# Performance work log

Hardware: AMD Instinct MI355X
Metric: run time of the kernel (lower is better)

The kernel has to match this reference:

```python
import jax, jax.numpy as jnp
import numpy as np

V, H, I, E, K, L = 32000, 1024, 4096, 8, 2, 2
B, S = 1, 2048

def setup_inputs() -> dict:
    key = jax.random.key(0)
    ks = jax.random.split(key, 8)
    s = 0.02
    d = {}
    d["input_ids"] = jax.random.randint(ks[0], (B, S), 0, V)
    d["emb"] = jax.random.normal(ks[1], (V, H), jnp.float32) * s
    d["router_w"] = jax.random.normal(ks[2], (L, E, H), jnp.float32) * s
    d["router_b"] = jnp.zeros((L, E), jnp.float32)
    d["fc1_w"] = jax.random.normal(ks[3], (L, E, I, H), jnp.float32) * s
    d["fc1_b"] = jnp.zeros((L, E, I), jnp.float32)
    d["fc2_w"] = jax.random.normal(ks[4], (L, E, H, I), jnp.float32) * s
    d["fc2_b"] = jnp.zeros((L, E, H), jnp.float32)
    d["ln_g"] = jnp.ones((L, H), jnp.float32)
    d["ln_b"] = jnp.zeros((L, H), jnp.float32)
    d["head_w"] = jax.random.normal(ks[5], (V, H), jnp.float32) * s
    d["head_b"] = jnp.zeros((V,), jnp.float32)
    return d

def _moe_layer(h, rw, rb, f1w, f1b, f2w, f2b, g, b):
    # h: [T,H]
    T = h.shape[0]
    logits = h @ rw.T + rb                                  # [T,E]
    top_w, sel = jax.lax.top_k(logits, K)                   # [T,K]
    top_w = jax.nn.softmax(top_w, axis=-1)
    sel_oh = sel[None, :, :] == jnp.arange(E)[:, None, None]  # [E,T,K]
    mask = sel_oh.any(-1)                                     # [E,T]
    w_tok = jnp.sum(jnp.where(sel_oh, top_w[None], 0.0), -1)  # [E,T]
    cnt = mask.sum(-1).astype(h.dtype)                        # [E]
    # faithful to source: per-expert SCALAR weight = mean of routing weights of routed tokens
    scal = jnp.where(cnt > 0, w_tok.sum(-1) / jnp.maximum(cnt, 1.0), 0.0)  # [E]
    a = jax.nn.gelu(jnp.einsum('th,eih->eti', h, f1w) + f1b[:, None, :], approximate=False)
    eo = jnp.einsum('eti,ehi->eth', a, f2w) + f2b[:, None, :]             # [E,T,H]
    out = jnp.einsum('et,eth->th', mask.astype(h.dtype) * scal[:, None], eo)
    mu = out.mean(-1, keepdims=True)
    var = out.var(-1, keepdims=True)
    out = (out - mu) / jnp.sqrt(var + 1e-5) * g + b
    counts = sel_oh.sum((1, 2)).astype(h.dtype)
    aux = jnp.mean((counts - T / E) ** 2) * 0.01
    return out, aux

def reference(input_ids, emb, router_w, router_b, fc1_w, fc1_b, fc2_w, fc2_b, ln_g, ln_b, head_w, head_b):
    h = emb[input_ids].reshape(-1, H)   # [T,H]
    aux_total = jnp.float32(0.0)
    for l in range(L):
        h, aux = _moe_layer(h, router_w[l], router_b[l], fc1_w[l], fc1_b[l],
                            fc2_w[l], fc2_b[l], ln_g[l], ln_b[l])
        aux_total = aux_total + aux
    logits = h @ head_w.T + head_b
    return logits.reshape(B, S, V), aux_total
```

## Files before the change

### kernel.cpp

```cpp
#include <hip/hip_runtime.h>
#include <math.h>

constexpr int kT = 2048;
constexpr int kH = 1024;
constexpr int kI = 4096;
constexpr int kE = 8;
constexpr int kV = 32000;
constexpr int kL = 2;
constexpr int kR = 4096;
constexpr int kRp = 5120;
constexpr int kSK = 4;
constexpr int kNB = kR / 128 + kE - 1;

typedef __attribute__((ext_vector_type(4))) float f32x4;
typedef __attribute__((ext_vector_type(8))) short bf16x8;

__device__ inline unsigned cvtpk(float lo, float hi) {
  unsigned r;
  asm("v_cvt_pk_bf16_f32 %0, %1, %2" : "=v"(r) : "v"(lo), "v"(hi));
  return r;
}

__device__ inline unsigned short f2bf(float x) {
  union { float f; unsigned u; } c; c.f = x;
  unsigned u = c.u;
  u += 0x7FFFu + ((u >> 16) & 1u);
  return (unsigned short)(u >> 16);
}

__device__ inline void dec2(float x, float y,
                            unsigned& p1, unsigned& p2, unsigned& p3) {
  unsigned ux = __float_as_uint(x), uy = __float_as_uint(y);
  unsigned x1 = ux & 0xFFFF0000u, y1 = uy & 0xFFFF0000u;
  float rx = x - __uint_as_float(x1), ry = y - __uint_as_float(y1);
  unsigned x2 = __float_as_uint(rx) & 0xFFFF0000u;
  unsigned y2 = __float_as_uint(ry) & 0xFFFF0000u;
  float sx = rx - __uint_as_float(x2), sy = ry - __uint_as_float(y2);
  p1 = (x1 >> 16) | y1;
  p2 = (x2 >> 16) | y2;
  p3 = (__float_as_uint(sx) >> 16) | (__float_as_uint(sy) & 0xFFFF0000u);
}

__device__ inline void dec1(float x, unsigned short& b1, unsigned short& b2,
                            unsigned short& b3) {
  unsigned u = __float_as_uint(x);
  unsigned x1 = u & 0xFFFF0000u;
  float r = x - __uint_as_float(x1);
  unsigned x2 = __float_as_uint(r) & 0xFFFF0000u;
  float s = r - __uint_as_float(x2);
  b1 = (unsigned short)(x1 >> 16);
  b2 = (unsigned short)(x2 >> 16);
  b3 = (unsigned short)(__float_as_uint(s) >> 16);
}

__device__ inline int swz(int e) { return e ^ (((e >> 6) & 3) << 3); }


__global__ void gather_k(const int* __restrict__ ids, const float* __restrict__ emb,
                         float* __restrict__ h) {
  int t = blockIdx.x;
  int id = ids[t];
  const float4* src = (const float4*)(emb + (size_t)id * kH);
  float4* dst = (float4*)(h + (size_t)t * kH);
  dst[threadIdx.x] = src[threadIdx.x];
}

__global__ void router_k(const float* __restrict__ h, const float* __restrict__ rw,
                         const float* __restrict__ rb, float* __restrict__ logits) {
  int t = blockIdx.x;
  int lg = threadIdx.x & 31;
  int e = threadIdx.x >> 5;
  const float* hr = h + (size_t)t * kH;
  const float* wr = rw + (size_t)e * kH;
  float p = 0.f;
  for (int k = lg * 4; k < kH; k += 128) {
    float4 a = *(const float4*)(hr + k);
    float4 b = *(const float4*)(wr + k);
    p += a.x * b.x + a.y * b.y + a.z * b.z + a.w * b.w;
  }
  for (int o = 16; o > 0; o >>= 1) p += __shfl_down(p, o, 32);
  if (lg == 0) logits[t * kE + e] = p + rb[e];
}

__global__ void topk_k(const float* __restrict__ logits, int* __restrict__ sel,
                       float* __restrict__ w_sum, int* __restrict__ cnt) {
  int t = blockIdx.x * blockDim.x + threadIdx.x;
  if (t >= kT) return;
  float v[8];
#pragma unroll
  for (int e = 0; e < 8; e++) v[e] = logits[t * 8 + e];
  int e1 = 0; float v1 = v[0];
#pragma unroll
  for (int e = 1; e < 8; e++) if (v[e] > v1) { v1 = v[e]; e1 = e; }
  int e2 = -1; float v2 = -3.4e38f;
#pragma unroll
  for (int e = 0; e < 8; e++) if (e != e1 && v[e] > v2) { v2 = v[e]; e2 = e; }
  float z = expf(v2 - v1);
  float w1 = 1.f / (1.f + z);
  float w2 = z * w1;
  sel[t * 2] = e1;
  sel[t * 2 + 1] = e2;
  atomicAdd(&w_sum[e1], w1);
  atomicAdd(&w_sum[e2], w2);
  atomicAdd(&cnt[e1], 1);
  atomicAdd(&cnt[e2], 1);
}

__global__ void finalize_k(const int* __restrict__ cnt, const float* __restrict__ w_sum,
                           float* __restrict__ scal, int* __restrict__ off,
                           int* __restrict__ fill, float* __restrict__ aux,
                           int* __restrict__ blk_e, int* __restrict__ blk_m) {
  if (threadIdx.x == 0) {
    int o = 0;
    float a = 0.f;
    for (int e = 0; e < 8; e++) {
      off[e] = o;
      o += (cnt[e] + 127) & ~127;
      fill[e] = 0;
      int c = cnt[e];
      scal[e] = c > 0 ? w_sum[e] / (float)c : 0.f;
      float d = (float)c - 256.f;
      a += d * d;
    }
    aux[0] += 0.01f * (a * 0.125f);
    int nb = 0;
    for (int e = 0; e < 8; e++)
      for (int m = 0; m < cnt[e]; m += 128) { blk_e[nb] = e; blk_m[nb] = m; nb++; }
    for (int i = nb; i < kNB; i++) { blk_e[i] = -1; blk_m[i] = 0; }
  }
}

__global__ void scatter_k(const int* __restrict__ sel, const int* __restrict__ off,
                          int* __restrict__ fill, int* __restrict__ list,
                          int* __restrict__ pos) {
  int t = blockIdx.x * blockDim.x + threadIdx.x;
  if (t >= kT) return;
#pragma unroll
  for (int s = 0; s < 2; s++) {
    int e = sel[t * 2 + s];
    int p = atomicAdd(&fill[e], 1);
    int slot = off[e] + p;
    list[slot] = t;
    pos[t * 2 + s] = slot;
  }
}

__global__ void cvt_k(const float* __restrict__ src, unsigned short* __restrict__ dst, long n) {
  long i = ((long)blockIdx.x * 256 + threadIdx.x) * 8;
  if (i >= n) return;
  float4 a = *(const float4*)(src + i);
  float4 b = *(const float4*)(src + i + 4);
  uint4 pk;
  pk.x = (unsigned)f2bf(a.x) | ((unsigned)f2bf(a.y) << 16);
  pk.y = (unsigned)f2bf(a.z) | ((unsigned)f2bf(a.w) << 16);
  pk.z = (unsigned)f2bf(b.x) | ((unsigned)f2bf(b.y) << 16);
  pk.w = (unsigned)f2bf(b.z) | ((unsigned)f2bf(b.w) << 16);
  *(uint4*)(dst + i) = pk;
}

__global__ void hdec_k(const float* __restrict__ h, const int* __restrict__ list,
                       unsigned short* __restrict__ hp, long PH) {
  int s = blockIdx.x * 2 + (threadIdx.x >> 7);
  int k8 = (threadIdx.x & 127) * 8;
  int t = list[s];
  const float* src = h + (size_t)t * kH + k8;
  float4 a = *(const float4*)(src);
  float4 b = *(const float4*)(src + 4);
  float x[8];
  *(float4*)&x[0] = a; *(float4*)&x[4] = b;
  unsigned q1[4], q2[4], q3[4];
#pragma unroll
  for (int i = 0; i < 4; i++) dec2(x[2 * i], x[2 * i + 1], q1[i], q2[i], q3[i]);
  int sw = (s >> 1) & 3;
  int colp = (k8 & ~31) | ((((k8 >> 3) & 3) ^ sw) << 3);
  long base = (long)s * kH + colp;
  *(uint4*)(hp + 0 * PH + base) = *(uint4*)q1;
  *(uint4*)(hp + 1 * PH + base) = *(uint4*)q2;
  *(uint4*)(hp + 2 * PH + base) = *(uint4*)q3;
}

__global__ void combine_ln_k(const float* __restrict__ ccomp, const int* __restrict__ pos,
                             float* __restrict__ h, const float* __restrict__ g,
                             const float* __restrict__ b) {
  int t = blockIdx.x;
  int s0 = pos[t * 2], s1 = pos[t * 2 + 1];
  int k = threadIdx.x * 4;
  float4 v = {0.f, 0.f, 0.f, 0.f};
#pragma unroll
  for (int kc = 0; kc < kSK; kc++) {
    const float* base = ccomp + (size_t)kc * ((size_t)kRp * kH);
    float4 a = *(const float4*)(base + (size_t)s0 * kH + k);
    float4 c = *(const float4*)(base + (size_t)s1 * kH + k);
    v.x += a.x + c.x; v.y += a.y + c.y; v.z += a.z + c.z; v.w += a.w + c.w;
  }
  float s = v.x + v.y + v.z + v.w;
  float sq = v.x * v.x + v.y * v.y + v.z * v.z + v.w * v.w;
  for (int o = 32; o > 0; o >>= 1) {
    s += __shfl_down(s, o);
    sq += __shfl_down(sq, o);
  }
  __shared__ float ss[4], sqs[4];
  int wave = threadIdx.x >> 6, lane = threadIdx.x & 63;
  if (lane == 0) { ss[wave] = s; sqs[wave] = sq; }
  __syncthreads();
  __shared__ float mu, inv;
  if (threadIdx.x == 0) {
    float st = ss[0] + ss[1] + ss[2] + ss[3];
    float sqt = sqs[0] + sqs[1] + sqs[2] + sqs[3];
    float m = st / (float)kH;
    float var = sqt / (float)kH - m * m;
    mu = m;
    inv = 1.f / sqrtf(var + 1e-5f);
  }
  __syncthreads();
  float4 gg = *(const float4*)(g + k);
  float4 bb = *(const float4*)(b + k);
  float4 o;
  o.x = (v.x - mu) * inv * gg.x + bb.x;
  o.y = (v.y - mu) * inv * gg.y + bb.y;
  o.z = (v.z - mu) * inv * gg.z + bb.z;
  o.w = (v.w - mu) * inv * gg.w + bb.w;
  *(float4*)(h + (size_t)t * kH + k) = o;
}

__global__ void aux_write_k(float* __restrict__ out, const float* __restrict__ aux) {
  out[(size_t)kT * kV] = aux[0];
}

template <int MODE>
__launch_bounds__(256)
__global__ void tgemm_k(const unsigned short* __restrict__ Ap, long PA, int ldA,
                        const float* __restrict__ Bbase,
                        const float* __restrict__ bias,
                        float* __restrict__ Cout,
                        unsigned short* __restrict__ Cp, long PCp,
                        const int* __restrict__ off,
                        const int* __restrict__ cnt,
                        const float* __restrict__ scal,
                        const int* __restrict__ blk_e,
                        const int* __restrict__ blk_m,
                        int N, int Kd) {
  const int e = blk_e[blockIdx.y];
  if (e < 0) return;
  const int m0 = blk_m[blockIdx.y];
  const int M = cnt[e];
  int nb = blockIdx.x, kc = 0;
  if constexpr (MODE == 1) { nb = blockIdx.x >> 2; kc = blockIdx.x & 3; }
  const int n0 = nb * 128;
  const int roff = off[e];
  const float* Bp = Bbase + (size_t)e * (size_t)N * (size_t)Kd;
  const float* be = bias + (size_t)e * (size_t)N;
  const int kBeg = (MODE == 1) ? kc * (Kd >> 2) : 0;
  const int kEnd = (MODE == 1) ? kBeg + (Kd >> 2) : Kd;

  __shared__ __align__(16) unsigned short AsL[2][3][128 * 32];
  __shared__ __align__(16) unsigned short BsL[3][128 * 32];

  const int tid = threadIdx.x, w = tid >> 6, l = tid & 63;

  long abase[2];
#pragma unroll
  for (int i = 0; i < 2; i++) {
    int r = w * 16 + i * 64 + (l >> 2);
    int gr = m0 + r; if (gr > M - 1) gr = M - 1;
    abase[i] = (long)(roff + gr) * ldA + (l & 3) * 8;
  }

  const int srow = tid >> 1, scolh = (tid & 1) * 16;
  const float* bsrc = Bp + (size_t)(n0 + srow) * (size_t)Kd + scolh;
  const int e0 = srow * 32 + scolh;
  const int s0b = swz(e0), s1b = swz(e0 + 8);

  f32x4 acc[4][4] = {};
  const int wm = w >> 1, wn = w & 1;
  const int fr = l & 15, fk = (l >> 4) * 8;
  const int cola = ((l >> 4) ^ ((fr >> 1) & 3)) * 8;

  float4 rvb[4];
  unsigned qb1[8], qb2[8], qb3[8];

#define LOADB(K0)                                      \
  _Pragma("unroll") for (int i = 0; i < 4; i++)        \
    rvb[i] = *(const float4*)(bsrc + (K0) + i * 4);

#define DECB()                                                 \
  {                                                            \
    float xb[16];                                              \
    *(float4*)&xb[0] = rvb[0]; *(float4*)&xb[4] = rvb[1];      \
    *(float4*)&xb[8] = rvb[2]; *(float4*)&xb[12] = rvb[3];     \
    _Pragma("unroll") for (int i = 0; i < 8; i++)              \
      dec2(xb[2 * i], xb[2 * i + 1], qb1[i], qb2[i], qb3[i]);  \
  }

#define ISSUE_A(K0, PBUF)                                                      \
  _Pragma("unroll") for (int pp = 0; pp < 3; pp++)                             \
    _Pragma("unroll") for (int ii = 0; ii < 2; ii++)                           \
      __builtin_amdgcn_global_load_lds(                                        \
          (const __attribute__((address_space(1))) unsigned int*)(const void*) \
              (Ap + (long)pp * PA + abase[ii] + (K0)),                         \
          (__attribute__((address_space(3))) unsigned int*)(void*)             \
              (&AsL[PBUF][pp][(w * 16 + ii * 64) * 32]),                       \
          16, 0, 0);

  LOADB(kBeg);
  DECB();
  ISSUE_A(kBeg, 0);
  int p = 0;

  for (int k0 = kBeg; k0 < kEnd; k0 += 32) {
    *(uint4*)&BsL[0][s0b] = *(uint4*)&qb1[0]; *(uint4*)&BsL[0][s1b] = *(uint4*)&qb1[4];
    *(uint4*)&BsL[1][s0b] = *(uint4*)&qb2[0]; *(uint4*)&BsL[1][s1b] = *(uint4*)&qb2[4];
    *(uint4*)&BsL[2][s0b] = *(uint4*)&qb3[0]; *(uint4*)&BsL[2][s1b] = *(uint4*)&qb3[4];
    __syncthreads();
    const bool more = (k0 + 32 < kEnd);
    if (more) {
      ISSUE_A(k0 + 32, (p ^ 1));
      LOADB(k0 + 32);
    }

    bf16x8 bf1[4], bf2[4], bf3[4];
#pragma unroll
    for (int bn = 0; bn < 4; bn++) {
      int se = swz((wn * 64 + bn * 16 + fr) * 32 + fk);
      bf1[bn] = *(const bf16x8*)(&BsL[0][se]);
      bf2[bn] = *(const bf16x8*)(&BsL[1][se]);
      bf3[bn] = *(const bf16x8*)(&BsL[2][se]);
    }
#pragma unroll
    for (int am = 0; am < 4; am++) {
      int ra = (wm * 64 + am * 16 + fr) * 32 + cola;
      bf16x8 a1 = *(const bf16x8*)(&AsL[p][0][ra]);
      bf16x8 a2 = *(const bf16x8*)(&AsL[p][1][ra]);
      bf16x8 a3 = *(const bf16x8*)(&AsL[p][2][ra]);
#pragma unroll
      for (int bn = 0; bn < 4; bn++) {
        f32x4 c = acc[am][bn];
        c = __builtin_amdgcn_mfma_f32_16x16x32_bf16(a3, bf1[bn], c, 0, 0, 0);
        c = __builtin_amdgcn_mfma_f32_16x16x32_bf16(a2, bf2[bn], c, 0, 0, 0);
        c = __builtin_amdgcn_mfma_f32_16x16x32_bf16(a1, bf3[bn], c, 0, 0, 0);
        c = __builtin_amdgcn_mfma_f32_16x16x32_bf16(a2, bf1[bn], c, 0, 0, 0);
        c = __builtin_amdgcn_mfma_f32_16x16x32_bf16(a1, bf2[bn], c, 0, 0, 0);
        c = __builtin_amdgcn_mfma_f32_16x16x32_bf16(a1, bf1[bn], c, 0, 0, 0);
        acc[am][bn] = c;
      }
    }
    if (more) DECB();
    __syncthreads();
    p ^= 1;
  }
#undef LOADB
#undef DECB
#undef ISSUE_A

  const int r0 = (l >> 4) * 4, cc = l & 15;
#pragma unroll
  for (int am = 0; am < 4; am++) {
#pragma unroll
    for (int bn = 0; bn < 4; bn++) {
      int gn = n0 + wn * 64 + bn * 16 + cc;
      float bv;
      if constexpr (MODE == 1) bv = (kc == 0) ? be[gn] : 0.f;
      else bv = be[gn];
#pragma unroll
      for (int j = 0; j < 4; j++) {
        int gm = m0 + wm * 64 + am * 16 + r0 + j;
        if (gm >= M) continue;
        float v = acc[am][bn][j] + bv;
        if constexpr (MODE == 0) {
          float g = 0.5f * v * (1.f + erff(v * 0.70710678118654752f));
          unsigned short b1, b2, b3;
          dec1(g, b1, b2, b3);
          int sw2 = ((r0 + j) >> 1) & 3;
          int colp = (gn & ~31) | ((((gn >> 3) & 3) ^ sw2) << 3) | (gn & 7);
          long base = (long)(roff + gm) * N + colp;
          Cp[0 * PCp + base] = b1;
          Cp[1 * PCp + base] = b2;
          Cp[2 * PCp + base] = b3;
        } else {
          Cout[(size_t)kc * ((size_t)kRp * kH) + (size_t)(roff + gm) * (size_t)N + gn] =
              scal[e] * v;
        }
      }
    }
  }
}

template <int MODE>
__launch_bounds__(256)
__global__ void wgemm_k(const unsigned short* __restrict__ Abase, int ldA,
                        const unsigned short* __restrict__ Bbase,
                        const float* __restrict__ bias,
                        float* __restrict__ Cout,
                        unsigned short* __restrict__ Cbf,
                        const int* __restrict__ list,
                        const int* __restrict__ off,
                        const int* __restrict__ cnt,
                        const float* __restrict__ scal,
                        const int* __restrict__ blk_e,
                        const int* __restrict__ blk_m,
                        int N, int Kd) {
  const int e = blk_e[blockIdx.x];
  if (e < 0) return;
  const int m0 = blk_m[blockIdx.x];
  const int M = cnt[e];
  int nb = blockIdx.y, kc = 0;
  if constexpr (MODE == 1) { nb = blockIdx.y >> 2; kc = blockIdx.y & 3; }
  const int n0 = nb * 128;
  const int roff = off[e];
  const unsigned short* Bp = Bbase + (size_t)e * (size_t)N * (size_t)Kd;
  const float* be = bias + (size_t)e * (size_t)N;
  const int kBeg = (MODE == 1) ? kc * (Kd >> 2) : 0;
  const int kEnd = (MODE == 1) ? kBeg + (Kd >> 2) : Kd;

  __shared__ __align__(16) unsigned short As[128 * 64];
  __shared__ __align__(16) unsigned short Bs[128 * 64];

  const int tid = threadIdx.x, w = tid >> 6, l = tid & 63;

  const unsigned short* asrc[4];
  const unsigned short* bsrc[4];
#pragma unroll
  for (int i = 0; i < 4; i++) {
    int r = w * 8 + i * 32 + (l >> 3);
    int gr = m0 + r; if (gr > M - 1) gr = M - 1;
    long grow;
    if constexpr (MODE == 0) grow = list[roff + gr];
    else grow = roff + gr;
    asrc[i] = Abase + grow * (long)ldA + (l & 7) * 8;
    bsrc[i] = Bp + (size_t)(n0 + r) * (size_t)Kd + (l & 7) * 8;
  }

  f32x4 acc[4][4] = {};
  const int wm = w >> 1, wn = w & 1;
  const int fr = l & 15, fk = (l >> 4) * 8;

  for (int k0 = kBeg; k0 < kEnd; k0 += 64) {
#pragma unroll
    for (int i = 0; i < 4; i++) {
      __builtin_amdgcn_global_load_lds(
          (const __attribute__((address_space(1))) unsigned int*)(const void*)(asrc[i] + k0),
          (__attribute__((address_space(3))) unsigned int*)(void*)(As + w * 512 + i * 2048),
          16, 0, 0);
      __builtin_amdgcn_global_load_lds(
          (const __attribute__((address_space(1))) unsigned int*)(const void*)(bsrc[i] + k0),
          (__attribute__((address_space(3))) unsigned int*)(void*)(Bs + w * 512 + i * 2048),
          16, 0, 0);
    }
    __syncthreads();
#pragma unroll
    for (int ks = 0; ks < 2; ks++) {
      bf16x8 af[4], bfr[4];
#pragma unroll
      for (int am = 0; am < 4; am++)
        af[am] = *(const bf16x8*)(As + (wm * 64 + am * 16 + fr) * 64 + ks * 32 + fk);
#pragma unroll
      for (int bn = 0; bn < 4; bn++)
        bfr[bn] = *(const bf16x8*)(Bs + (wn * 64 + bn * 16 + fr) * 64 + ks * 32 + fk);
#pragma unroll
      for (int am = 0; am < 4; am++)
#pragma unroll
        for (int bn = 0; bn < 4; bn++)
          acc[am][bn] = __builtin_amdgcn_mfma_f32_16x16x32_bf16(af[am], bfr[bn], acc[am][bn], 0, 0, 0);
    }
    __syncthreads();
  }

  const int r0 = (l >> 4) * 4, cc = l & 15;
#pragma unroll
  for (int am = 0; am < 4; am++) {
#pragma unroll
    for (int bn = 0; bn < 4; bn++) {
      int gn = n0 + wn * 64 + bn * 16 + cc;
      float bv;
      if constexpr (MODE == 1) bv = (kc == 0) ? be[gn] : 0.f;
      else bv = be[gn];
#pragma unroll
      for (int j = 0; j < 4; j++) {
        int gm = m0 + wm * 64 + am * 16 + r0 + j;
        if (gm >= M) continue;
        float v = acc[am][bn][j] + bv;
        if constexpr (MODE == 0) {
          float g = 0.5f * v * (1.f + erff(v * 0.70710678118654752f));
          Cbf[(size_t)(roff + gm) * (size_t)N + gn] = f2bf(g);
        } else {
          Cout[(size_t)kc * ((size_t)kRp * kH) + (size_t)(roff + gm) * (size_t)N + gn] =
              scal[e] * v;
        }
      }
    }
  }
}

__launch_bounds__(256)
__global__ void hgemm_k(const unsigned short* __restrict__ hbf,
                        const float* __restrict__ Bw,
                        const float* __restrict__ bias,
                        float* __restrict__ Cout) {
  int bx = blockIdx.x, by = blockIdx.y;
  {
    int lin = by * gridDim.x + bx;
    int nwg = gridDim.x * gridDim.y;
    int q = nwg >> 3, r = nwg & 7;
    int xcd = lin & 7, idx = lin >> 3;
    int swzb = (xcd < r ? xcd * (q + 1) : r * (q + 1) + (xcd - r) * q) + idx;
    bx = swzb % gridDim.x;
    by = swzb / gridDim.x;
  }
  const int m0 = bx * 128;
  const int n0 = by * 128;

  __shared__ __align__(16) unsigned short As[128 * 64];
  __shared__ __align__(16) unsigned short Bs[128 * 64];

  const int tid = threadIdx.x, w = tid >> 6, l = tid & 63;

  const unsigned short* asrc[4];
  const float* bsrc[4];
#pragma unroll
  for (int i = 0; i < 4; i++) {
    int r = w * 8 + i * 32 + (l >> 3);
    asrc[i] = hbf + (size_t)(m0 + r) * kH + (l & 7) * 8;
    bsrc[i] = Bw + (size_t)(n0 + r) * kH + (l & 7) * 8;
  }
  const int ldstB = w * 512 + (l >> 3) * 64 + (((l & 7) ^ (l >> 3)) * 8);

  f32x4 acc[4][4] = {};
  const int wm = w >> 1, wn = w & 1;
  const int fr = l & 15, fk = (l >> 4) * 8;
  const int col0 = (((l >> 4) + 0) ^ (l & 7)) * 8;
  const int col1 = (((l >> 4) + 4) ^ (l & 7)) * 8;

  float4 rb[4][2];
#define LOADB(K0)                                            \
  _Pragma("unroll") for (int i = 0; i < 4; i++) {            \
    rb[i][0] = *(const float4*)(bsrc[i] + (K0));             \
    rb[i][1] = *(const float4*)(bsrc[i] + (K0) + 4);         \
  }

  LOADB(0);

  for (int k0 = 0; k0 < kH; k0 += 64) {
#pragma unroll
    for (int i = 0; i < 4; i++) {
      __builtin_amdgcn_global_load_lds(
          (const __attribute__((address_space(1))) unsigned int*)(const void*)(asrc[i] + k0),
          (__attribute__((address_space(3))) unsigned int*)(void*)(As + w * 512 + i * 2048),
          16, 0, 0);
      uint4 pb;
      pb.x = cvtpk(rb[i][0].x, rb[i][0].y);
      pb.y = cvtpk(rb[i][0].z, rb[i][0].w);
      pb.z = cvtpk(rb[i][1].x, rb[i][1].y);
      pb.w = cvtpk(rb[i][1].z, rb[i][1].w);
      *(uint4*)(Bs + ldstB + i * 2048) = pb;
    }
    __syncthreads();
    if (k0 + 64 < kH) LOADB(k0 + 64);
#pragma unroll
    for (int ks = 0; ks < 2; ks++) {
      const int ck = ks ? col1 : col0;
      bf16x8 af[4], bfr[4];
#pragma unroll
      for (int am = 0; am < 4; am++)
        af[am] = *(const bf16x8*)(As + (wm * 64 + am * 16 + fr) * 64 + ks * 32 + fk);
#pragma unroll
      for (int bn = 0; bn < 4; bn++)
        bfr[bn] = *(const bf16x8*)(Bs + (wn * 64 + bn * 16 + fr) * 64 + ck);
#pragma unroll
      for (int am = 0; am < 4; am++)
#pragma unroll
        for (int bn = 0; bn < 4; bn++)
          acc[am][bn] = __builtin_amdgcn_mfma_f32_16x16x32_bf16(af[am], bfr[bn], acc[am][bn], 0, 0, 0);
    }
    __syncthreads();
  }
#undef LOADB

  const int r0 = (l >> 4) * 4, cc = l & 15;
#pragma unroll
  for (int am = 0; am < 4; am++) {
#pragma unroll
    for (int bn = 0; bn < 4; bn++) {
      int gn = n0 + wn * 64 + bn * 16 + cc;
      float bv = bias[gn];
#pragma unroll
      for (int j = 0; j < 4; j++) {
        int gm = m0 + wm * 64 + am * 16 + r0 + j;
        Cout[(size_t)gm * (size_t)kV + gn] = acc[am][bn][j] + bv;
      }
    }
  }
}


extern "C" void kernel_launch(void* const* d_in, const int* in_sizes, int n_in,
                              void* d_out, int out_size, void* d_ws, size_t ws_size,
                              hipStream_t stream) {
  (void)in_sizes; (void)n_in; (void)out_size; (void)ws_size;
  const int* ids = (const int*)d_in[0];
  const float* emb = (const float*)d_in[1];
  const float* router_w = (const float*)d_in[2];
  const float* router_b = (const float*)d_in[3];
  const float* fc1_w = (const float*)d_in[4];
  const float* fc1_b = (const float*)d_in[5];
  const float* fc2_w = (const float*)d_in[6];
  const float* fc2_b = (const float*)d_in[7];
  const float* ln_g = (const float*)d_in[8];
  const float* ln_b = (const float*)d_in[9];
  const float* head_w = (const float*)d_in[10];
  const float* head_b = (const float*)d_in[11];
  float* out = (float*)d_out;

  float* ws_f = (float*)d_ws;
  float* h       = ws_f;
  float* logits  = h + (size_t)kT * kH;
  float* w_sum   = logits + (size_t)kT * kE;
  float* scal    = w_sum + kE;
  float* aux     = scal + kE;
  int* sel  = (int*)(aux + 1);
  int* cnt  = sel + 2 * kT;
  int* off  = cnt + kE;
  int* fill = off + kE;
  int* list = fill + kE;
  int* pos  = list + kRp;
  int* blk_e = pos + 2 * kT;
  int* blk_m = blk_e + kNB;
  unsigned short* h_bf = (unsigned short*)(blk_m + kNB);

  const long PA_h = (long)kRp * kH;
  const long PA_a = (long)kRp * kI;
  unsigned short* ap = (unsigned short*)out;
  unsigned short* hp = ap + 3 * PA_a;
  float* c_comp = (float*)(hp + 3 * PA_h);
  unsigned short* a_bf = (unsigned short*)out;
  unsigned short* wbf = a_bf + (size_t)kRp * kI;

  hipMemsetAsync(aux, 0, sizeof(float), stream);
  gather_k<<<kT, 256, 0, stream>>>(ids, emb, h);

  for (int l = 0; l < kL; l++) {
    hipMemsetAsync(w_sum, 0, kE * sizeof(float), stream);
    hipMemsetAsync(cnt, 0, kE * sizeof(int), stream);
    hipMemsetAsync(list, 0, kRp * sizeof(int), stream);
    router_k<<<kT, 256, 0, stream>>>(h, router_w + (size_t)l * kE * kH,
                                     router_b + (size_t)l * kE, logits);
    topk_k<<<kT / 256, 256, 0, stream>>>(logits, sel, w_sum, cnt);
    finalize_k<<<1, 64, 0, stream>>>(cnt, w_sum, scal, off, fill, aux, blk_e, blk_m);
    scatter_k<<<kT / 256, 256, 0, stream>>>(sel, off, fill, list, pos);

    if (l == 0) {
      hdec_k<<<kRp / 2, 256, 0, stream>>>(h, list, hp, PA_h);
      tgemm_k<0><<<dim3(kI / 128, kNB), 256, 0, stream>>>(
          hp, PA_h, kH, fc1_w + (size_t)l * kE * kI * kH, fc1_b + (size_t)l * kE * kI,
          nullptr, ap, PA_a, off, cnt, scal, blk_e, blk_m, kI, kH);
      tgemm_k<1><<<dim3((kH / 128) * kSK, kNB), 256, 0, stream>>>(
          ap, PA_a, kI, fc2_w + (size_t)l * kE * kH * kI, fc2_b + (size_t)l * kE * kH,
          c_comp, nullptr, 0, off, cnt, scal, blk_e, blk_m, kH, kI);
    } else {
      cvt_k<<<(int)(((long)kT * kH) / 2048), 256, 0, stream>>>(h, h_bf, (long)kT * kH);
      cvt_k<<<(int)(((long)kE * kI * kH) / 2048), 256, 0, stream>>>(
          fc1_w + (size_t)l * kE * kI * kH, wbf, (long)kE * kI * kH);
      wgemm_k<0><<<dim3(kNB, kI / 128), 256, 0, stream>>>(
          h_bf, kH, wbf, fc1_b + (size_t)l * kE * kI,
          nullptr, a_bf, list, off, cnt, scal, blk_e, blk_m, kI, kH);
      cvt_k<<<(int)(((long)kE * kH * kI) / 2048), 256, 0, stream>>>(
          fc2_w + (size_t)l * kE * kH * kI, wbf, (long)kE * kH * kI);
      wgemm_k<1><<<dim3(kNB, (kH / 128) * kSK), 256, 0, stream>>>(
          a_bf, kI, wbf, fc2_b + (size_t)l * kE * kH,
          c_comp, nullptr, list, off, cnt, scal, blk_e, blk_m, kH, kI);
    }

    combine_ln_k<<<kT, 256, 0, stream>>>(c_comp, pos, h,
                                         ln_g + (size_t)l * kH, ln_b + (size_t)l * kH);
  }

  cvt_k<<<(int)(((long)kT * kH) / 2048), 256, 0, stream>>>(h, h_bf, (long)kT * kH);
  hgemm_k<<<dim3(kT / 128, kV / 128), 256, 0, stream>>>(h_bf, head_w, head_b, out);

  aux_write_k<<<1, 1, 0, stream>>>(out, aux);
}
```

Measured before the change: 1.396 ms.

## Fuse bf16 output into LayerNorm and add bf16-weight head GEMM

The combine+LayerNorm kernel now also writes a bf16 copy of the hidden state, which removes the separate float-to-bf16 conversion kernels before the layer-1 FC1 and before the LM head. When the workspace is large enough, the head weight is converted to bf16 once per call. A new head GEMM then streams both operands in bf16 through global_load_lds into LDS with XCD-aware block swizzling. This trades an extra pass over the 128MB fp32 head weight for half-width operand traffic in the main GEMM. The new path depends on ws_size, and the old hgemm_k path is kept as a fallback.

```diff
diff --git a/kernel.cpp b/kernel.cpp
--- a/kernel.cpp
+++ b/kernel.cpp
@@ -180,8 +180,8 @@
 }
 
 __global__ void combine_ln_k(const float* __restrict__ ccomp, const int* __restrict__ pos,
-                             float* __restrict__ h, const float* __restrict__ g,
-                             const float* __restrict__ b) {
+                             float* __restrict__ h, unsigned short* __restrict__ hbf,
+                             const float* __restrict__ g, const float* __restrict__ b) {
   int t = blockIdx.x;
   int s0 = pos[t * 2], s1 = pos[t * 2 + 1];
   int k = threadIdx.x * 4;
@@ -221,6 +221,10 @@
   o.z = (v.z - mu) * inv * gg.z + bb.z;
   o.w = (v.w - mu) * inv * gg.w + bb.w;
   *(float4*)(h + (size_t)t * kH + k) = o;
+  uint2 pk;
+  pk.x = (unsigned)f2bf(o.x) | ((unsigned)f2bf(o.y) << 16);
+  pk.y = (unsigned)f2bf(o.z) | ((unsigned)f2bf(o.w) << 16);
+  *(uint2*)(hbf + (size_t)t * kH + k) = pk;
 }
 
 __global__ void aux_write_k(float* __restrict__ out, const float* __restrict__ aux) {
@@ -591,11 +595,94 @@
   }
 }
 
+__launch_bounds__(256)
+__global__ void hgemm2_k(const unsigned short* __restrict__ hbf,
+                         const unsigned short* __restrict__ Bw,
+                         const float* __restrict__ bias,
+                         float* __restrict__ Cout) {
+  int bx = blockIdx.x, by = blockIdx.y;
+  {
+    int lin = by * gridDim.x + bx;
+    int nwg = gridDim.x * gridDim.y;
+    int q = nwg >> 3, r = nwg & 7;
+    int xcd = lin & 7, idx = lin >> 3;
+    int swzb = (xcd < r ? xcd * (q + 1) : r * (q + 1) + (xcd - r) * q) + idx;
+    bx = swzb % gridDim.x;
+    by = swzb / gridDim.x;
+  }
+  const int m0 = bx * 128;
+  const int n0 = by * 128;
+
+  __shared__ __align__(16) unsigned short As[128 * 64];
+  __shared__ __align__(16) unsigned short Bs[128 * 64];
+
+  const int tid = threadIdx.x, w = tid >> 6, l = tid & 63;
+
+  const unsigned short* asrc[4];
+  const unsigned short* bsrc[4];
+#pragma unroll
+  for (int i = 0; i < 4; i++) {
+    int r = w * 8 + i * 32 + (l >> 3);
+    asrc[i] = hbf + (size_t)(m0 + r) * kH + (l & 7) * 8;
+    bsrc[i] = Bw + (size_t)(n0 + r) * kH + (l & 7) * 8;
+  }
+
+  f32x4 acc[4][4] = {};
+  const int wm = w >> 1, wn = w & 1;
+  const int fr = l & 15, fk = (l >> 4) * 8;
+
+  for (int k0 = 0; k0 < kH; k0 += 64) {
+#pragma unroll
+    for (int i = 0; i < 4; i++) {
+      __builtin_amdgcn_global_load_lds(
+          (const __attribute__((address_space(1))) unsigned int*)(const void*)(asrc[i] + k0),
+          (__attribute__((address_space(3))) unsigned int*)(void*)(As + w * 512 + i * 2048),
+          16, 0, 0);
+      __builtin_amdgcn_global_load_lds(
+          (const __attribute__((address_space(1))) unsigned int*)(const void*)(bsrc[i] + k0),
+          (__attribute__((address_space(3))) unsigned int*)(void*)(Bs + w * 512 + i * 2048),
+          16, 0, 0);
+    }
+    __syncthreads();
+#pragma unroll
+    for (int ks = 0; ks < 2; ks++) {
+      bf16x8 af[4], bfr[4];
+#pragma unroll
+      for (int am = 0; am < 4; am++)
+        af[am] = *(const bf16x8*)(As + (wm * 64 + am * 16 + fr) * 64 + ks * 32 + fk);
+#pragma unroll
+      for (int bn = 0; bn < 4; bn++)
+        bfr[bn] = *(const bf16x8*)(Bs + (wn * 64 + bn * 16 + fr) * 64 + ks * 32 + fk);
+#pragma unroll
+      for (int am = 0; am < 4; am++)
+#pragma unroll
+        for (int bn = 0; bn < 4; bn++)
+          acc[am][bn] = __builtin_amdgcn_mfma_f32_16x16x32_bf16(af[am], bfr[bn], acc[am][bn], 0, 0, 0);
+    }
+    __syncthreads();
+  }
+
+  const int r0 = (l >> 4) * 4, cc = l & 15;
+#pragma unroll
+  for (int am = 0; am < 4; am++) {
+#pragma unroll
+    for (int bn = 0; bn < 4; bn++) {
+      int gn = n0 + wn * 64 + bn * 16 + cc;
+      float bv = bias[gn];
+#pragma unroll
+      for (int j = 0; j < 4; j++) {
+        int gm = m0 + wm * 64 + am * 16 + r0 + j;
+        Cout[(size_t)gm * (size_t)kV + gn] = acc[am][bn][j] + bv;
+      }
+    }
+  }
+}
+
 
 extern "C" void kernel_launch(void* const* d_in, const int* in_sizes, int n_in,
                               void* d_out, int out_size, void* d_ws, size_t ws_size,
                               hipStream_t stream) {
-  (void)in_sizes; (void)n_in; (void)out_size; (void)ws_size;
+  (void)in_sizes; (void)n_in; (void)out_size;
   const int* ids = (const int*)d_in[0];
   const float* emb = (const float*)d_in[1];
   const float* router_w = (const float*)d_in[2];
@@ -625,6 +712,9 @@
   int* blk_e = pos + 2 * kT;
   int* blk_m = blk_e + kNB;
   unsigned short* h_bf = (unsigned short*)(blk_m + kNB);
+  unsigned short* hw_bf = h_bf + (size_t)kT * kH;
+  size_t ws_need = ((char*)(hw_bf + (size_t)kV * kH) - (char*)d_ws);
+  bool head_bf = ws_size >= ws_need;
 
   const long PA_h = (long)kRp * kH;
   const long PA_a = (long)kRp * kI;
@@ -656,7 +746,6 @@
           ap, PA_a, kI, fc2_w + (size_t)l * kE * kH * kI, fc2_b + (size_t)l * kE * kH,
           c_comp, nullptr, 0, off, cnt, scal, blk_e, blk_m, kH, kI);
     } else {
-      cvt_k<<<(int)(((long)kT * kH) / 2048), 256, 0, stream>>>(h, h_bf, (long)kT * kH);
       cvt_k<<<(int)(((long)kE * kI * kH) / 2048), 256, 0, stream>>>(
           fc1_w + (size_t)l * kE * kI * kH, wbf, (long)kE * kI * kH);
       wgemm_k<0><<<dim3(kNB, kI / 128), 256, 0, stream>>>(
@@ -669,12 +758,16 @@
           c_comp, nullptr, list, off, cnt, scal, blk_e, blk_m, kH, kI);
     }
 
-    combine_ln_k<<<kT, 256, 0, stream>>>(c_comp, pos, h,
+    combine_ln_k<<<kT, 256, 0, stream>>>(c_comp, pos, h, h_bf,
                                          ln_g + (size_t)l * kH, ln_b + (size_t)l * kH);
   }
 
-  cvt_k<<<(int)(((long)kT * kH) / 2048), 256, 0, stream>>>(h, h_bf, (long)kT * kH);
-  hgemm_k<<<dim3(kT / 128, kV / 128), 256, 0, stream>>>(h_bf, head_w, head_b, out);
+  if (head_bf) {
+    cvt_k<<<(int)(((long)kV * kH) / 2048), 256, 0, stream>>>(head_w, hw_bf, (long)kV * kH);
+    hgemm2_k<<<dim3(kT / 128, kV / 128), 256, 0, stream>>>(h_bf, hw_bf, head_b, out);
+  } else {
+    hgemm_k<<<dim3(kT / 128, kV / 128), 256, 0, stream>>>(h_bf, head_w, head_b, out);
+  }
 
   aux_write_k<<<1, 1, 0, stream>>>(out, aux);
 }
```

After: 1.459 ms. 4.5% more time.

## Load A fragments directly from global in tgemm and fuse bf16 cast into layernorm

Applied to the files above, without the earlier changes.

The split-bf16 GEMM (tgemm) no longer stages A tiles through LDS with async global_load_lds double buffering. Each lane now reads its A fragments straight from global memory into registers, and the swizzled column layout used by the producers of hp and ap is dropped to match. Separately, combine_ln_k now also writes a bf16 copy of h, which removes two cvt_k launches. Direct global A loads cut LDS traffic and occupancy pressure, but they add uncoalesced, latency-exposed global reads inside the MFMA loop with no prefetch.

```diff
diff --git a/kernel.cpp b/kernel.cpp
--- a/kernel.cpp
+++ b/kernel.cpp
@@ -171,17 +171,15 @@
   unsigned q1[4], q2[4], q3[4];
 #pragma unroll
   for (int i = 0; i < 4; i++) dec2(x[2 * i], x[2 * i + 1], q1[i], q2[i], q3[i]);
-  int sw = (s >> 1) & 3;
-  int colp = (k8 & ~31) | ((((k8 >> 3) & 3) ^ sw) << 3);
-  long base = (long)s * kH + colp;
+  long base = (long)s * kH + k8;
   *(uint4*)(hp + 0 * PH + base) = *(uint4*)q1;
   *(uint4*)(hp + 1 * PH + base) = *(uint4*)q2;
   *(uint4*)(hp + 2 * PH + base) = *(uint4*)q3;
 }
 
 __global__ void combine_ln_k(const float* __restrict__ ccomp, const int* __restrict__ pos,
-                             float* __restrict__ h, const float* __restrict__ g,
-                             const float* __restrict__ b) {
+                             float* __restrict__ h, unsigned short* __restrict__ hbf,
+                             const float* __restrict__ g, const float* __restrict__ b) {
   int t = blockIdx.x;
   int s0 = pos[t * 2], s1 = pos[t * 2 + 1];
   int k = threadIdx.x * 4;
@@ -221,6 +219,10 @@
   o.z = (v.z - mu) * inv * gg.z + bb.z;
   o.w = (v.w - mu) * inv * gg.w + bb.w;
   *(float4*)(h + (size_t)t * kH + k) = o;
+  uint2 pk;
+  pk.x = (unsigned)f2bf(o.x) | ((unsigned)f2bf(o.y) << 16);
+  pk.y = (unsigned)f2bf(o.z) | ((unsigned)f2bf(o.w) << 16);
+  *(uint2*)(hbf + (size_t)t * kH + k) = pk;
 }
 
 __global__ void aux_write_k(float* __restrict__ out, const float* __restrict__ aux) {
@@ -253,17 +255,19 @@
   const int kBeg = (MODE == 1) ? kc * (Kd >> 2) : 0;
   const int kEnd = (MODE == 1) ? kBeg + (Kd >> 2) : Kd;
 
-  __shared__ __align__(16) unsigned short AsL[2][3][128 * 32];
   __shared__ __align__(16) unsigned short BsL[3][128 * 32];
 
   const int tid = threadIdx.x, w = tid >> 6, l = tid & 63;
 
-  long abase[2];
-#pragma unroll
-  for (int i = 0; i < 2; i++) {
-    int r = w * 16 + i * 64 + (l >> 2);
-    int gr = m0 + r; if (gr > M - 1) gr = M - 1;
-    abase[i] = (long)(roff + gr) * ldA + (l & 3) * 8;
+  const int wm = w >> 1, wn = w & 1;
+  const int fr = l & 15, fk = (l >> 4) * 8;
+
+  const unsigned short* aptr[4];
+#pragma unroll
+  for (int am = 0; am < 4; am++) {
+    int gr = m0 + wm * 64 + am * 16 + fr;
+    if (gr > M - 1) gr = M - 1;
+    aptr[am] = Ap + (long)(roff + gr) * ldA + fk;
   }
 
   const int srow = tid >> 1, scolh = (tid & 1) * 16;
@@ -272,9 +276,6 @@
   const int s0b = swz(e0), s1b = swz(e0 + 8);
 
   f32x4 acc[4][4] = {};
-  const int wm = w >> 1, wn = w & 1;
-  const int fr = l & 15, fk = (l >> 4) * 8;
-  const int cola = ((l >> 4) ^ ((fr >> 1) & 3)) * 8;
 
   float4 rvb[4];
   unsigned qb1[8], qb2[8], qb3[8];
@@ -292,20 +293,8 @@
       dec2(xb[2 * i], xb[2 * i + 1], qb1[i], qb2[i], qb3[i]);  \
   }
 
-#define ISSUE_A(K0, PBUF)                                                      \
-  _Pragma("unroll") for (int pp = 0; pp < 3; pp++)                             \
-    _Pragma("unroll") for (int ii = 0; ii < 2; ii++)                           \
-      __builtin_amdgcn_global_load_lds(                                        \
-          (const __attribute__((address_space(1))) unsigned int*)(const void*) \
-              (Ap + (long)pp * PA + abase[ii] + (K0)),                         \
-          (__attribute__((address_space(3))) unsigned int*)(void*)             \
-              (&AsL[PBUF][pp][(w * 16 + ii * 64) * 32]),                       \
-          16, 0, 0);
-
   LOADB(kBeg);
   DECB();
-  ISSUE_A(kBeg, 0);
-  int p = 0;
 
   for (int k0 = kBeg; k0 < kEnd; k0 += 32) {
     *(uint4*)&BsL[0][s0b] = *(uint4*)&qb1[0]; *(uint4*)&BsL[0][s1b] = *(uint4*)&qb1[4];
@@ -313,9 +302,14 @@
     *(uint4*)&BsL[2][s0b] = *(uint4*)&qb3[0]; *(uint4*)&BsL[2][s1b] = *(uint4*)&qb3[4];
     __syncthreads();
     const bool more = (k0 + 32 < kEnd);
-    if (more) {
-      ISSUE_A(k0 + 32, (p ^ 1));
-      LOADB(k0 + 32);
+    if (more) LOADB(k0 + 32);
+
+    bf16x8 af1[4], af2[4], af3[4];
+#pragma unroll
+    for (int am = 0; am < 4; am++) {
+      af1[am] = *(const bf16x8*)(aptr[am] + k0);
+      af2[am] = *(const bf16x8*)(aptr[am] + PA + k0);
+      af3[am] = *(const bf16x8*)(aptr[am] + 2 * PA + k0);
     }
 
     bf16x8 bf1[4], bf2[4], bf3[4];
@@ -328,29 +322,23 @@
     }
 #pragma unroll
     for (int am = 0; am < 4; am++) {
-      int ra = (wm * 64 + am * 16 + fr) * 32 + cola;
-      bf16x8 a1 = *(const bf16x8*)(&AsL[p][0][ra]);
-      bf16x8 a2 = *(const bf16x8*)(&AsL[p][1][ra]);
-      bf16x8 a3 = *(const bf16x8*)(&AsL[p][2][ra]);
 #pragma unroll
       for (int bn = 0; bn < 4; bn++) {
         f32x4 c = acc[am][bn];
-        c = __builtin_amdgcn_mfma_f32_16x16x32_bf16(a3, bf1[bn], c, 0, 0, 0);
-        c = __builtin_amdgcn_mfma_f32_16x16x32_bf16(a2, bf2[bn], c, 0, 0, 0);
-        c = __builtin_amdgcn_mfma_f32_16x16x32_bf16(a1, bf3[bn], c, 0, 0, 0);
-        c = __builtin_amdgcn_mfma_f32_16x16x32_bf16(a2, bf1[bn], c, 0, 0, 0);
-        c = __builtin_amdgcn_mfma_f32_16x16x32_bf16(a1, bf2[bn], c, 0, 0, 0);
-        c = __builtin_amdgcn_mfma_f32_16x16x32_bf16(a1, bf1[bn], c, 0, 0, 0);
+        c = __builtin_amdgcn_mfma_f32_16x16x32_bf16(af3[am], bf1[bn], c, 0, 0, 0);
+        c = __builtin_amdgcn_mfma_f32_16x16x32_bf16(af2[am], bf2[bn], c, 0, 0, 0);
+        c = __builtin_amdgcn_mfma_f32_16x16x32_bf16(af1[am], bf3[bn], c, 0, 0, 0);
+        c = __builtin_amdgcn_mfma_f32_16x16x32_bf16(af2[am], bf1[bn], c, 0, 0, 0);
+        c = __builtin_amdgcn_mfma_f32_16x16x32_bf16(af1[am], bf2[bn], c, 0, 0, 0);
+        c = __builtin_amdgcn_mfma_f32_16x16x32_bf16(af1[am], bf1[bn], c, 0, 0, 0);
         acc[am][bn] = c;
       }
     }
     if (more) DECB();
     __syncthreads();
-    p ^= 1;
   }
 #undef LOADB
 #undef DECB
-#undef ISSUE_A
 
   const int r0 = (l >> 4) * 4, cc = l & 15;
 #pragma unroll
@@ -370,9 +358,7 @@
           float g = 0.5f * v * (1.f + erff(v * 0.70710678118654752f));
           unsigned short b1, b2, b3;
           dec1(g, b1, b2, b3);
-          int sw2 = ((r0 + j) >> 1) & 3;
-          int colp = (gn & ~31) | ((((gn >> 3) & 3) ^ sw2) << 3) | (gn & 7);
-          long base = (long)(roff + gm) * N + colp;
+          long base = (long)(roff + gm) * N + gn;
           Cp[0 * PCp + base] = b1;
           Cp[1 * PCp + base] = b2;
           Cp[2 * PCp + base] = b3;
@@ -656,7 +642,6 @@
           ap, PA_a, kI, fc2_w + (size_t)l * kE * kH * kI, fc2_b + (size_t)l * kE * kH,
           c_comp, nullptr, 0, off, cnt, scal, blk_e, blk_m, kH, kI);
     } else {
-      cvt_k<<<(int)(((long)kT * kH) / 2048), 256, 0, stream>>>(h, h_bf, (long)kT * kH);
       cvt_k<<<(int)(((long)kE * kI * kH) / 2048), 256, 0, stream>>>(
           fc1_w + (size_t)l * kE * kI * kH, wbf, (long)kE * kI * kH);
       wgemm_k<0><<<dim3(kNB, kI / 128), 256, 0, stream>>>(
@@ -669,11 +654,10 @@
           c_comp, nullptr, list, off, cnt, scal, blk_e, blk_m, kH, kI);
     }
 
-    combine_ln_k<<<kT, 256, 0, stream>>>(c_comp, pos, h,
+    combine_ln_k<<<kT, 256, 0, stream>>>(c_comp, pos, h, h_bf,
                                          ln_g + (size_t)l * kH, ln_b + (size_t)l * kH);
   }
 
-  cvt_k<<<(int)(((long)kT * kH) / 2048), 256, 0, stream>>>(h, h_bf, (long)kT * kH);
   hgemm_k<<<dim3(kT / 128, kV / 128), 256, 0, stream>>>(h_bf, head_w, head_b, out);
 
   aux_write_k<<<1, 1, 0, stream>>>(out, aux);
```

After: 1.486 ms. +6.5%, slower.
